# Optimization experiments

Hardware: AMD Instinct MI355X
Metric: run time of the kernel (lower is better)

The kernel has to match this reference:

```python
import jax, jax.numpy as jnp
import numpy as np

NEG_INF = -1e30  # finite stand-in for log(0); keeps grads NaN-free

T_, B_, V_, L_ = 1024, 64, 512, 256


def setup_inputs() -> dict:
    key = jax.random.key(0)
    k1, k2 = jax.random.split(key)
    acts = jax.random.normal(k1, (T_, B_, V_), dtype=jnp.float32)
    labels = jax.random.randint(k2, (B_ * L_,), 1, V_, dtype=jnp.int32)  # blank=0 excluded
    act_lens = jnp.full((B_,), T_, dtype=jnp.int32)
    label_lens = jnp.full((B_,), L_, dtype=jnp.int32)
    return {"acts": acts, "labels": labels, "act_lens": act_lens, "label_lens": label_lens}


def _ctc_total_loss(acts, labels, act_lens, label_lens):
    # acts: (T, B, V) raw logits; warp-ctc applies softmax internally.
    T, B, V = acts.shape
    L = labels.shape[0] // B          # static max label length (uniform lengths)
    S = 2 * L + 1                     # extended label lattice with interleaved blanks
    logp = jax.nn.log_softmax(acts, axis=-1)

    # Unflatten labels -> padded (B, L)
    offsets = jnp.concatenate([jnp.zeros((1,), jnp.int32),
                               jnp.cumsum(label_lens.astype(jnp.int32))])[:-1]
    j = jnp.arange(L, dtype=jnp.int32)
    gidx = jnp.clip(offsets[:, None] + j[None, :], 0, labels.shape[0] - 1)
    padded = jnp.where(j[None, :] < label_lens[:, None], labels[gidx], 0)  # (B, L)

    # Extended labels: blank, l1, blank, l2, ..., blank
    ext = jnp.zeros((B, S), dtype=labels.dtype).at[:, 1::2].set(padded)
    ext_m2 = jnp.pad(ext, ((0, 0), (2, 0)))[:, :S]
    allow_skip = (ext != 0) & (ext != ext_m2)
    allow_skip = allow_skip.at[:, :2].set(False)

    bidx = jnp.arange(B)[:, None]
    lp_ext = logp[:, bidx, ext]       # (T, B, S): per-frame log-prob of lattice states

    alpha0 = jnp.full((B, S), NEG_INF, dtype=acts.dtype)
    alpha0 = alpha0.at[:, 0].set(lp_ext[0, :, 0]).at[:, 1].set(lp_ext[0, :, 1])
    neg = jnp.full((B, 1), NEG_INF, dtype=acts.dtype)

    def step(alpha, inp):
        lp_t, t = inp
        a1 = alpha
        a2 = jnp.concatenate([neg, alpha[:, :-1]], axis=1)
        a3 = jnp.concatenate([neg, neg, alpha[:, :-2]], axis=1)
        a3 = jnp.where(allow_skip, a3, NEG_INF)
        new = lp_t + jnp.logaddexp(jnp.logaddexp(a1, a2), a3)
        alpha = jnp.where((t < act_lens)[:, None], new, alpha)  # freeze past act_len
        return alpha, None

    alpha, _ = jax.lax.scan(step, alpha0, (lp_ext[1:], jnp.arange(1, T)))

    s_end = (2 * label_lens).astype(jnp.int32)           # final blank state
    a_end = jnp.take_along_axis(alpha, s_end[:, None], axis=1)[:, 0]
    a_end2 = jnp.take_along_axis(alpha, jnp.maximum(s_end - 1, 0)[:, None], axis=1)[:, 0]
    losses = -jnp.logaddexp(a_end, a_end2)               # per-example NLL
    return jnp.sum(losses)[None]                         # shape (1,), matches FloatTensor([sum])


def reference(acts, labels, act_lens, label_lens):
    return _ctc_total_loss(acts, labels, act_lens, label_lens)
```

## Files before the change

kernel.cpp:

```cpp
#include <hip/hip_runtime.h>

constexpr int T = 1024;
constexpr int B = 64;
constexpr int V = 512;
constexpr int L = 256;
constexpr int S = 2 * L + 1;
constexpr int C = 16;

typedef float f32x4 __attribute__((ext_vector_type(4)));

__device__ __forceinline__ unsigned short f2bf(float f) {
    unsigned u = __float_as_uint(f);
    u += 0x7fffu + ((u >> 16) & 1u);
    return (unsigned short)(u >> 16);
}


__global__ __launch_bounds__(64) void offsets_kernel(
    const int* __restrict__ label_lens, int* __restrict__ offsets)
{
    int lane = threadIdx.x;
    int v = (lane < B) ? label_lens[lane] : 0;
    int x = v;
#pragma unroll
    for (int o = 1; o < 64; o <<= 1) {
        int y = __shfl_up(x, o, 64);
        if (lane >= o) x += y;
    }
    if (lane < B) offsets[lane] = x - v;
}

__global__ __launch_bounds__(256) void setup_kernel(
    const float* __restrict__ acts, const int* __restrict__ labels,
    const int* __restrict__ label_lens, const int* __restrict__ offsets,
    float* __restrict__ lse_rows, unsigned short* __restrict__ packedU,
    float* __restrict__ blankU)
{
    __shared__ float rows[4][2][V];
    const int w    = threadIdx.x >> 6;
    const int lane = threadIdx.x & 63;
    const int rbase = (blockIdx.x * 4 + w) * 2;
    const f32x4* p = (const f32x4*)(acts + (size_t)rbase * V);

    f32x4 xa0 = __builtin_nontemporal_load(p + lane);
    f32x4 xa1 = __builtin_nontemporal_load(p + lane + 64);
    f32x4 xb0 = __builtin_nontemporal_load(p + lane + 128);
    f32x4 xb1 = __builtin_nontemporal_load(p + lane + 192);
    f32x4 ea0, ea1, eb0, eb1;
    ea0.x=__expf(xa0.x); ea0.y=__expf(xa0.y); ea0.z=__expf(xa0.z); ea0.w=__expf(xa0.w);
    ea1.x=__expf(xa1.x); ea1.y=__expf(xa1.y); ea1.z=__expf(xa1.z); ea1.w=__expf(xa1.w);
    eb0.x=__expf(xb0.x); eb0.y=__expf(xb0.y); eb0.z=__expf(xb0.z); eb0.w=__expf(xb0.w);
    eb1.x=__expf(xb1.x); eb1.y=__expf(xb1.y); eb1.z=__expf(xb1.z); eb1.w=__expf(xb1.w);
    ((f32x4*)rows[w][0])[lane]      = ea0;
    ((f32x4*)rows[w][0])[lane + 64] = ea1;
    ((f32x4*)rows[w][1])[lane]      = eb0;
    ((f32x4*)rows[w][1])[lane + 64] = eb1;
    float sa = ea0.x+ea0.y+ea0.z+ea0.w + ea1.x+ea1.y+ea1.z+ea1.w;
    float sb = eb0.x+eb0.y+eb0.z+eb0.w + eb1.x+eb1.y+eb1.z+eb1.w;
#pragma unroll
    for (int o = 32; o; o >>= 1) { sa += __shfl_xor(sa, o, 64); sb += __shfl_xor(sb, o, 64); }

#pragma unroll
    for (int rr = 0; rr < 2; ++rr) {
        const int r = rbase + rr;
        const int b = r & (B - 1), t = r >> 6;
        const float* rw = rows[w][rr];
        const int lab_len = label_lens[b];
        const int off     = offsets[b];
        const float ubk   = rw[0];
        const int j0 = 4 * lane;
        float q0 = (j0 + 0 < lab_len) ? rw[labels[min(off + j0 + 0, B * L - 1)]] : ubk;
        float q1 = (j0 + 1 < lab_len) ? rw[labels[min(off + j0 + 1, B * L - 1)]] : ubk;
        float q2 = (j0 + 2 < lab_len) ? rw[labels[min(off + j0 + 2, B * L - 1)]] : ubk;
        float q3 = (j0 + 3 < lab_len) ? rw[labels[min(off + j0 + 3, B * L - 1)]] : ubk;
        ushort4 hv = {f2bf(q0), f2bf(q1), f2bf(q2), f2bf(q3)};
        ((ushort4*)packedU)[(size_t)(b * T + t) * 64 + lane] = hv;
        if (lane == 0) {
            lse_rows[b * T + t] = __logf(rr ? sb : sa);
            blankU[b * T + t]   = ubk;
        }
    }
}

__global__ __launch_bounds__(128, 1) void ctc_kernel(
    const int* __restrict__ labels, const int* __restrict__ act_lens,
    const int* __restrict__ label_lens, const int* __restrict__ offsets,
    const float* __restrict__ lse_rows, const unsigned short* __restrict__ packedU,
    const float* __restrict__ blankU, float* __restrict__ out)
{
    __shared__ uint4 ubuf[2][2][C * 32];
    __shared__ float bbuf[2][2][C];
    __shared__ float sbr[S];
    __shared__ float s_accb;

    const int b    = blockIdx.x;
    const int wave = threadIdx.x >> 6;
    const int lane = threadIdx.x & 63;
    const int lab_len = label_lens[b];
    const int a_len   = act_lens[b];
    const int th      = (a_len - 1) >> 1;
    const int off     = offsets[b];
    const size_t rowbase = (size_t)b * T;

    int li0 = 4 * lane;
    int eprev = (li0 - 1 >= 0 && li0 - 1 < lab_len) ? labels[min(off + li0 - 1, B * L - 1)] : 0;
    int enext = (li0 + 4 < lab_len) ? labels[min(off + li0 + 4, B * L - 1)] : 0;
    int e0 = (li0 + 0 < lab_len) ? labels[min(off + li0 + 0, B * L - 1)] : 0;
    int e1 = (li0 + 1 < lab_len) ? labels[min(off + li0 + 1, B * L - 1)] : 0;
    int e2 = (li0 + 2 < lab_len) ? labels[min(off + li0 + 2, B * L - 1)] : 0;
    int e3 = (li0 + 3 < lab_len) ? labels[min(off + li0 + 3, B * L - 1)] : 0;

    const float aF0 = (8 * lane + 1 >= 2 && e0 != 0 && e0 != eprev) ? 1.f : 0.f;
    const float aF1 = (e1 != 0 && e1 != e0) ? 1.f : 0.f;
    const float aF2 = (e2 != 0 && e2 != e1) ? 1.f : 0.f;
    const float aF3 = (e3 != 0 && e3 != e2) ? 1.f : 0.f;
    const float aB0 = aF1, aB1 = aF2, aB2 = aF3;
    const float aB3 = (enext != 0 && enext != e3) ? 1.f : 0.f;

    float A0 = 0.f, A1 = 0.f, A2 = 0.f, A3 = 0.f, A4 = 0.f,
          A5 = 0.f, A6 = 0.f, A7 = 0.f, A8 = 0.f;
    float acc = 0.f, sls = 0.f;
    uint4 G0, G1, G2, G3, G4, G5, G6, G7;
    float BL = 0.f;

#define LOADCHUNK(TLO) do {                                                   \
        const uint4* gp_ = (const uint4*)(packedU + (rowbase + (TLO)) * 256); \
        G0 = gp_[lane];       G1 = gp_[lane + 64];                            \
        G2 = gp_[lane + 128]; G3 = gp_[lane + 192];                           \
        G4 = gp_[lane + 256]; G5 = gp_[lane + 320];                           \
        G6 = gp_[lane + 384]; G7 = gp_[lane + 448];                           \
        if (lane < C) BL = blankU[rowbase + (TLO) + lane];                    \
    } while (0)

#define WRITEBUF(BI) do {                                                     \
        uint4* wp_ = ubuf[wave][BI];                                          \
        wp_[lane] = G0;       wp_[lane + 64] = G1;                            \
        wp_[lane + 128] = G2; wp_[lane + 192] = G3;                           \
        wp_[lane + 256] = G4; wp_[lane + 320] = G5;                           \
        wp_[lane + 384] = G6; wp_[lane + 448] = G7;                           \
        if (lane < C) bbuf[wave][BI][lane] = BL;                              \
    } while (0)

#define RESCALE() do {                                                        \
        float m_ = fmaxf(A8, A0); m_ = fmaxf(m_, A1); m_ = fmaxf(m_, A2);     \
        m_ = fmaxf(m_, A3); m_ = fmaxf(m_, A4); m_ = fmaxf(m_, A5);           \
        m_ = fmaxf(m_, A6); m_ = fmaxf(m_, A7);                               \
        _Pragma("unroll")                                                     \
        for (int o_ = 32; o_; o_ >>= 1) m_ = fmaxf(m_, __shfl_xor(m_, o_, 64)); \
        m_ = fmaxf(m_, 1e-30f);                                               \
        float inv_ = __builtin_amdgcn_rcpf(m_);                               \
        acc += __logf(m_);                                                    \
        A0 *= inv_; A1 *= inv_; A2 *= inv_; A3 *= inv_; A4 *= inv_;           \
        A5 *= inv_; A6 *= inv_; A7 *= inv_; A8 *= inv_;                       \
    } while (0)

#define STEPF(BI, ROW) do {                                                   \
        uint2 hv_ = ((const uint2*)ubuf[wave][BI])[(ROW) * 64 + lane];        \
        float ub_ = bbuf[wave][BI][ROW];                                      \
        float u0_ = __uint_as_float(hv_.x << 16);                             \
        float u1_ = __uint_as_float(hv_.x & 0xffff0000u);                     \
        float u2_ = __uint_as_float(hv_.y << 16);                             \
        float u3_ = __uint_as_float(hv_.y & 0xffff0000u);                     \
        float pA7_ = __shfl_up(A7, 1, 64);                                    \
        if (lane == 0) pA7_ = 0.f;                                            \
        A8 = ub_ * (A8 + A7);                                                 \
        A7 = u3_ * fmaf(aF3, A5, A7 + A6);                                    \
        A6 = ub_ * (A6 + A5);                                                 \
        A5 = u2_ * fmaf(aF2, A3, A5 + A4);                                    \
        A4 = ub_ * (A4 + A3);                                                 \
        A3 = u1_ * fmaf(aF1, A1, A3 + A2);                                    \
        A2 = ub_ * (A2 + A1);                                                 \
        A1 = u0_ * fmaf(aF0, pA7_, A1 + A0);                                  \
        A0 = ub_ * (A0 + pA7_);                                               \
    } while (0)

#define STEPB(BI, ROW) do {                                                   \
        uint2 hv_ = ((const uint2*)ubuf[wave][BI])[(ROW) * 64 + lane];        \
        float ub_ = bbuf[wave][BI][ROW];                                      \
        float u0_ = __uint_as_float(hv_.x << 16);                             \
        float u1_ = __uint_as_float(hv_.x & 0xffff0000u);                     \
        float u2_ = __uint_as_float(hv_.y << 16);                             \
        float u3_ = __uint_as_float(hv_.y & 0xffff0000u);                     \
        float nB0_ = __shfl_down(A0, 1, 64);                                  \
        float nB1_ = __shfl_down(A1, 1, 64);                                  \
        if (lane == 63) { nB0_ = A8; nB1_ = 0.f; }                            \
        A8 = ub_ * A8;                                                        \
        A0 = ub_ * (A0 + A1);                                                 \
        A1 = u0_ * fmaf(aB0, A3, A1 + A2);                                    \
        A2 = ub_ * (A2 + A3);                                                 \
        A3 = u1_ * fmaf(aB1, A5, A3 + A4);                                    \
        A4 = ub_ * (A4 + A5);                                                 \
        A5 = u2_ * fmaf(aB2, A7, A5 + A6);                                    \
        A6 = ub_ * (A6 + A7);                                                 \
        A7 = u3_ * fmaf(aB3, nB1_, A7 + nB0_);                                \
    } while (0)

    if (wave == 0) {
        for (int t = lane; t < a_len; t += 64) sls += lse_rows[rowbase + t];
#pragma unroll
        for (int o = 32; o; o >>= 1) sls += __shfl_xor(sls, o, 64);

        if (lane == 0) {
            A0 = blankU[rowbase];
            A1 = __uint_as_float(((unsigned)packedU[rowbase * 256]) << 16);
        }

        const int nst = th;
        if (nst > 0) {
            const int nc = (nst + C - 1) / C;
            LOADCHUNK(1);
            WRITEBUF(0);
            LOADCHUNK(1 + C * min(1, nc - 1));
            for (int k = 0; k < nc; ++k) {
                const int bi  = k & 1;
                const int tlo = 1 + C * k;
#pragma unroll
                for (int i = 0; i < C; ++i) {
                    if (tlo + i <= th) STEPF(bi, i);
                    if (i == 7 || i == 15) RESCALE();
                }
                WRITEBUF((k + 1) & 1);
                LOADCHUNK(1 + C * min(k + 2, nc - 1));
            }
        }
    } else {
        const int send = 2 * lab_len;
        {
            size_t rl = rowbase + (a_len - 1);
            float ubl = blankU[rl];
            float ue  = (lab_len > 0)
                      ? __uint_as_float(((unsigned)packedU[rl * 256 + (lab_len - 1)]) << 16)
                      : 0.f;
            int s0 = 8 * lane;
            A0 = (s0 + 0 == send) ? ubl : ((s0 + 0 == send - 1) ? ue : 0.f);
            A1 = (s0 + 1 == send) ? ubl : ((s0 + 1 == send - 1) ? ue : 0.f);
            A2 = (s0 + 2 == send) ? ubl : ((s0 + 2 == send - 1) ? ue : 0.f);
            A3 = (s0 + 3 == send) ? ubl : ((s0 + 3 == send - 1) ? ue : 0.f);
            A4 = (s0 + 4 == send) ? ubl : ((s0 + 4 == send - 1) ? ue : 0.f);
            A5 = (s0 + 5 == send) ? ubl : ((s0 + 5 == send - 1) ? ue : 0.f);
            A6 = (s0 + 6 == send) ? ubl : ((s0 + 6 == send - 1) ? ue : 0.f);
            A7 = (s0 + 7 == send) ? ubl : ((s0 + 7 == send - 1) ? ue : 0.f);
            A8 = (lane == 63 && send == 512) ? ubl : 0.f;
        }

        const int nst = a_len - 2 - th;
        if (nst > 0) {
            const int nc = (nst + C - 1) / C;
#define BTLO(K) max(a_len - 2 - C * (K) - (C - 1), 0)
            LOADCHUNK(BTLO(0));
            WRITEBUF(0);
            LOADCHUNK(BTLO(min(1, nc - 1)));
            for (int k = 0; k < nc; ++k) {
                const int bi   = k & 1;
                const int thi  = a_len - 2 - C * k;
                const int tloc = max(thi - (C - 1), 0);
#pragma unroll
                for (int i = 0; i < C; ++i) {
                    int tt = thi - i;
                    if (tt >= th + 1) STEPB(bi, tt - tloc);
                    if (i == 7 || i == 15) RESCALE();
                }
                WRITEBUF((k + 1) & 1);
                LOADCHUNK(BTLO(min(k + 2, nc - 1)));
            }
#undef BTLO
        }

        {
            float nB0 = __shfl_down(A0, 1, 64);
            float nB1 = __shfl_down(A1, 1, 64);
            if (lane == 63) { nB0 = A8; nB1 = 0.f; }
            float w0 = A0 + A1;
            float w1 = fmaf(aB0, A3, A1 + A2);
            float w2 = A2 + A3;
            float w3 = fmaf(aB1, A5, A3 + A4);
            float w4 = A4 + A5;
            float w5 = fmaf(aB2, A7, A5 + A6);
            float w6 = A6 + A7;
            float w7 = fmaf(aB3, nB1, A7 + nB0);
            int s0 = 8 * lane;
            sbr[s0 + 0] = w0; sbr[s0 + 1] = w1; sbr[s0 + 2] = w2; sbr[s0 + 3] = w3;
            sbr[s0 + 4] = w4; sbr[s0 + 5] = w5; sbr[s0 + 6] = w6; sbr[s0 + 7] = w7;
            if (lane == 63) sbr[512] = A8;
            if (lane == 0)  s_accb = acc;
        }
    }
    __syncthreads();
    if (wave == 0) {
        int s0 = 8 * lane;
        float p0 = __logf(fmaxf(A0, 1e-37f)) + __logf(fmaxf(sbr[s0 + 0], 1e-37f));
        float p1 = __logf(fmaxf(A1, 1e-37f)) + __logf(fmaxf(sbr[s0 + 1], 1e-37f));
        float p2 = __logf(fmaxf(A2, 1e-37f)) + __logf(fmaxf(sbr[s0 + 2], 1e-37f));
        float p3 = __logf(fmaxf(A3, 1e-37f)) + __logf(fmaxf(sbr[s0 + 3], 1e-37f));
        float p4 = __logf(fmaxf(A4, 1e-37f)) + __logf(fmaxf(sbr[s0 + 4], 1e-37f));
        float p5 = __logf(fmaxf(A5, 1e-37f)) + __logf(fmaxf(sbr[s0 + 5], 1e-37f));
        float p6 = __logf(fmaxf(A6, 1e-37f)) + __logf(fmaxf(sbr[s0 + 6], 1e-37f));
        float p7 = __logf(fmaxf(A7, 1e-37f)) + __logf(fmaxf(sbr[s0 + 7], 1e-37f));
        float p8 = -3.0e38f;
        if (lane == 63) p8 = __logf(fmaxf(A8, 1e-37f)) + __logf(fmaxf(sbr[512], 1e-37f));
        float pmax = fmaxf(fmaxf(fmaxf(p0, p1), fmaxf(p2, p3)),
                           fmaxf(fmaxf(p4, p5), fmaxf(p6, p7)));
        pmax = fmaxf(pmax, p8);
#pragma unroll
        for (int o = 32; o; o >>= 1) pmax = fmaxf(pmax, __shfl_xor(pmax, o, 64));
        float dot = __expf(p0 - pmax) + __expf(p1 - pmax) + __expf(p2 - pmax)
                  + __expf(p3 - pmax) + __expf(p4 - pmax) + __expf(p5 - pmax)
                  + __expf(p6 - pmax) + __expf(p7 - pmax);
        if (lane == 63) dot += __expf(p8 - pmax);
#pragma unroll
        for (int o = 32; o; o >>= 1) dot += __shfl_xor(dot, o, 64);
        if (lane == 0) {
            float loss = sls - acc - s_accb - (pmax + __logf(dot));
            atomicAdd(out, loss);
        }
    }
#undef LOADCHUNK
#undef WRITEBUF
#undef RESCALE
#undef STEPF
#undef STEPB
}

extern "C" void kernel_launch(void* const* d_in, const int* in_sizes, int n_in,
                              void* d_out, int out_size, void* d_ws, size_t ws_size,
                              hipStream_t stream) {
    const float* acts       = (const float*)d_in[0];
    const int*   labels     = (const int*)d_in[1];
    const int*   act_lens   = (const int*)d_in[2];
    const int*   label_lens = (const int*)d_in[3];
    float*       out        = (float*)d_out;

    float*          lse_rows = (float*)d_ws;
    float*          blankU   = (float*)((char*)d_ws + (size_t)T * B * 4);
    int*            offsets  = (int*)  ((char*)d_ws + (size_t)2 * T * B * 4);
    unsigned short* packedU  = (unsigned short*)((char*)d_ws + (1u << 20));

    hipMemsetAsync(d_out, 0, sizeof(float), stream);

    offsets_kernel<<<1, 64, 0, stream>>>(label_lens, offsets);
    setup_kernel<<<T * B / 8, 256, 0, stream>>>(
        acts, labels, label_lens, offsets, lse_rows, packedU, blankU);
    ctc_kernel<<<B, 128, 0, stream>>>(
        labels, act_lens, label_lens, offsets, lse_rows, packedU, blankU, out);
}
```

Baseline: 279.4 us.

## Stream CTC emission chunks through registers instead of LDS double buffer

Removes the shared-memory staging buffers. Each wave now loads 16-step chunks of packed bf16 emissions directly into two register arrays that ping-pong, and takes the blank probability from a lane via readlane instead of from LDS. The backward recursion's state layout is shifted by one so lane 0 holds the extra state. Chunks are fully unrolled with a remainder loop that reads global memory directly, and rescaling happens once per chunk instead of twice. This trades higher register pressure and extra edge-case complexity for fewer LDS writes and reads on the serial recurrence path.

```diff
diff --git a/kernel.cpp b/kernel.cpp
--- a/kernel.cpp
+++ b/kernel.cpp
@@ -13,6 +13,10 @@
     unsigned u = __float_as_uint(f);
     u += 0x7fffu + ((u >> 16) & 1u);
     return (unsigned short)(u >> 16);
+}
+
+__device__ __forceinline__ float lane_bcast(float v, int i) {
+    return __uint_as_float((unsigned)__builtin_amdgcn_readlane((int)__float_as_uint(v), i));
 }
 
 
@@ -88,8 +92,6 @@
     const float* __restrict__ lse_rows, const unsigned short* __restrict__ packedU,
     const float* __restrict__ blankU, float* __restrict__ out)
 {
-    __shared__ uint4 ubuf[2][2][C * 32];
-    __shared__ float bbuf[2][2][C];
     __shared__ float sbr[S];
     __shared__ float s_accb;
 
@@ -120,25 +122,16 @@
     float A0 = 0.f, A1 = 0.f, A2 = 0.f, A3 = 0.f, A4 = 0.f,
           A5 = 0.f, A6 = 0.f, A7 = 0.f, A8 = 0.f;
     float acc = 0.f, sls = 0.f;
-    uint4 G0, G1, G2, G3, G4, G5, G6, G7;
-    float BL = 0.f;
-
-#define LOADCHUNK(TLO) do {                                                   \
-        const uint4* gp_ = (const uint4*)(packedU + (rowbase + (TLO)) * 256); \
-        G0 = gp_[lane];       G1 = gp_[lane + 64];                            \
-        G2 = gp_[lane + 128]; G3 = gp_[lane + 192];                           \
-        G4 = gp_[lane + 256]; G5 = gp_[lane + 320];                           \
-        G6 = gp_[lane + 384]; G7 = gp_[lane + 448];                           \
-        if (lane < C) BL = blankU[rowbase + (TLO) + lane];                    \
-    } while (0)
-
-#define WRITEBUF(BI) do {                                                     \
-        uint4* wp_ = ubuf[wave][BI];                                          \
-        wp_[lane] = G0;       wp_[lane + 64] = G1;                            \
-        wp_[lane + 128] = G2; wp_[lane + 192] = G3;                           \
-        wp_[lane + 256] = G4; wp_[lane + 320] = G5;                           \
-        wp_[lane + 384] = G6; wp_[lane + 448] = G7;                           \
-        if (lane < C) bbuf[wave][BI][lane] = BL;                              \
+
+    uint2 Ua[C], Ub[C];
+    float Ka = 0.f, Kb = 0.f;
+
+#define LOADCH(U, K, TLO) do {                                                \
+        const int tl_ = min(max((int)(TLO), 0), T - C);                       \
+        const uint2* gp_ = (const uint2*)(packedU + (rowbase + tl_) * 256);   \
+        _Pragma("unroll")                                                     \
+        for (int i_ = 0; i_ < C; ++i_) U[i_] = gp_[i_ * 64 + lane];           \
+        K = blankU[rowbase + tl_ + (lane & (C - 1))];                         \
     } while (0)
 
 #define RESCALE() do {                                                        \
@@ -154,13 +147,13 @@
         A5 *= inv_; A6 *= inv_; A7 *= inv_; A8 *= inv_;                       \
     } while (0)
 
-#define STEPF(BI, ROW) do {                                                   \
-        uint2 hv_ = ((const uint2*)ubuf[wave][BI])[(ROW) * 64 + lane];        \
-        float ub_ = bbuf[wave][BI][ROW];                                      \
-        float u0_ = __uint_as_float(hv_.x << 16);                             \
-        float u1_ = __uint_as_float(hv_.x & 0xffff0000u);                     \
-        float u2_ = __uint_as_float(hv_.y << 16);                             \
-        float u3_ = __uint_as_float(hv_.y & 0xffff0000u);                     \
+#define STEPF_CORE(HX, HY, UB) do {                                           \
+        const float ub_ = (UB);                                               \
+        const unsigned hx_ = (HX), hy_ = (HY);                                \
+        const float u0_ = __uint_as_float(hx_ << 16);                         \
+        const float u1_ = __uint_as_float(hx_ & 0xffff0000u);                 \
+        const float u2_ = __uint_as_float(hy_ << 16);                         \
+        const float u3_ = __uint_as_float(hy_ & 0xffff0000u);                 \
         float pA7_ = __shfl_up(A7, 1, 64);                                    \
         if (lane == 0) pA7_ = 0.f;                                            \
         A8 = ub_ * (A8 + A7);                                                 \
@@ -173,26 +166,33 @@
         A1 = u0_ * fmaf(aF0, pA7_, A1 + A0);                                  \
         A0 = ub_ * (A0 + pA7_);                                               \
     } while (0)
-
-#define STEPB(BI, ROW) do {                                                   \
-        uint2 hv_ = ((const uint2*)ubuf[wave][BI])[(ROW) * 64 + lane];        \
-        float ub_ = bbuf[wave][BI][ROW];                                      \
-        float u0_ = __uint_as_float(hv_.x << 16);                             \
-        float u1_ = __uint_as_float(hv_.x & 0xffff0000u);                     \
-        float u2_ = __uint_as_float(hv_.y << 16);                             \
-        float u3_ = __uint_as_float(hv_.y & 0xffff0000u);                     \
-        float nB0_ = __shfl_down(A0, 1, 64);                                  \
-        float nB1_ = __shfl_down(A1, 1, 64);                                  \
-        if (lane == 63) { nB0_ = A8; nB1_ = 0.f; }                            \
-        A8 = ub_ * A8;                                                        \
-        A0 = ub_ * (A0 + A1);                                                 \
-        A1 = u0_ * fmaf(aB0, A3, A1 + A2);                                    \
-        A2 = ub_ * (A2 + A3);                                                 \
-        A3 = u1_ * fmaf(aB1, A5, A3 + A4);                                    \
-        A4 = ub_ * (A4 + A5);                                                 \
-        A5 = u2_ * fmaf(aB2, A7, A5 + A6);                                    \
-        A6 = ub_ * (A6 + A7);                                                 \
-        A7 = u3_ * fmaf(aB3, nB1_, A7 + nB0_);                                \
+#define STEPF_R(U, K, I) STEPF_CORE(U[I].x, U[I].y, lane_bcast(K, I))
+
+#define STEPB_CORE(HX, HY, UB) do {                                           \
+        const float ub_ = (UB);                                               \
+        const unsigned hx_ = (HX), hy_ = (HY);                                \
+        const float u0_ = __uint_as_float(hx_ << 16);                         \
+        const float u1_ = __uint_as_float(hx_ & 0xffff0000u);                 \
+        const float u2_ = __uint_as_float(hy_ << 16);                         \
+        const float u3_ = __uint_as_float(hy_ & 0xffff0000u);                 \
+        float nC0_ = __shfl_down(A0, 1, 64);                                  \
+        if (lane == 63) nC0_ = 0.f;                                           \
+        A8 = ub_ * (A8 + A0);                                                 \
+        A0 = u0_ * fmaf(aB0, A2, A0 + A1);                                    \
+        A1 = ub_ * (A1 + A2);                                                 \
+        A2 = u1_ * fmaf(aB1, A4, A2 + A3);                                    \
+        A3 = ub_ * (A3 + A4);                                                 \
+        A4 = u2_ * fmaf(aB2, A6, A4 + A5);                                    \
+        A5 = ub_ * (A5 + A6);                                                 \
+        A6 = u3_ * fmaf(aB3, nC0_, A6 + A7);                                  \
+        A7 = ub_ * (A7 + nC0_);                                               \
+    } while (0)
+#define STEPB_R(U, K, I) STEPB_CORE(U[I].x, U[I].y, lane_bcast(K, I))
+
+#define STEP_DIRECT(WHICH, TT) do {                                           \
+        uint2 hvd_ = ((const uint2*)(packedU + (rowbase + (TT)) * 256))[lane];\
+        float ubd_ = blankU[rowbase + (TT)];                                  \
+        WHICH(hvd_.x, hvd_.y, ubd_);                                          \
     } while (0)
 
     if (wave == 0) {
@@ -205,22 +205,34 @@
             A1 = __uint_as_float(((unsigned)packedU[rowbase * 256]) << 16);
         }
 
-        const int nst = th;
-        if (nst > 0) {
-            const int nc = (nst + C - 1) / C;
-            LOADCHUNK(1);
-            WRITEBUF(0);
-            LOADCHUNK(1 + C * min(1, nc - 1));
-            for (int k = 0; k < nc; ++k) {
-                const int bi  = k & 1;
-                const int tlo = 1 + C * k;
-#pragma unroll
-                for (int i = 0; i < C; ++i) {
-                    if (tlo + i <= th) STEPF(bi, i);
-                    if (i == 7 || i == 15) RESCALE();
-                }
-                WRITEBUF((k + 1) & 1);
-                LOADCHUNK(1 + C * min(k + 2, nc - 1));
+        if (th >= 1) {
+            const int kfull = (th - 15) >> 4;
+            LOADCH(Ua, Ka, 0);
+            LOADCH(Ub, Kb, 16);
+#pragma unroll
+            for (int i = 1; i < C; ++i) { if (i <= th) STEPF_R(Ua, Ka, i); }
+            RESCALE();
+            LOADCH(Ua, Ka, 32);
+            int k = 1;
+            for (; k + 1 <= kfull; k += 2) {
+#pragma unroll
+                for (int i = 0; i < C; ++i) STEPF_R(Ub, Kb, i);
+                RESCALE();
+                LOADCH(Ub, Kb, 16 * (k + 2));
+#pragma unroll
+                for (int i = 0; i < C; ++i) STEPF_R(Ua, Ka, i);
+                RESCALE();
+                LOADCH(Ua, Ka, 16 * (k + 3));
+            }
+            if (k <= kfull) {
+#pragma unroll
+                for (int i = 0; i < C; ++i) STEPF_R(Ub, Kb, i);
+                RESCALE();
+            }
+            const int tS = (kfull >= 1) ? 16 * (kfull + 1) : 16;
+            for (int t = tS; t <= th; ++t) {
+                STEP_DIRECT(STEPF_CORE, t);
+                if (((t - tS) & 7) == 7) RESCALE();
             }
         }
     } else {
@@ -231,7 +243,7 @@
             float ue  = (lab_len > 0)
                       ? __uint_as_float(((unsigned)packedU[rl * 256 + (lab_len - 1)]) << 16)
                       : 0.f;
-            int s0 = 8 * lane;
+            int s0 = 8 * lane + 1;
             A0 = (s0 + 0 == send) ? ubl : ((s0 + 0 == send - 1) ? ue : 0.f);
             A1 = (s0 + 1 == send) ? ubl : ((s0 + 1 == send - 1) ? ue : 0.f);
             A2 = (s0 + 2 == send) ? ubl : ((s0 + 2 == send - 1) ? ue : 0.f);
@@ -240,49 +252,65 @@
             A5 = (s0 + 5 == send) ? ubl : ((s0 + 5 == send - 1) ? ue : 0.f);
             A6 = (s0 + 6 == send) ? ubl : ((s0 + 6 == send - 1) ? ue : 0.f);
             A7 = (s0 + 7 == send) ? ubl : ((s0 + 7 == send - 1) ? ue : 0.f);
-            A8 = (lane == 63 && send == 512) ? ubl : 0.f;
-        }
-
-        const int nst = a_len - 2 - th;
-        if (nst > 0) {
-            const int nc = (nst + C - 1) / C;
-#define BTLO(K) max(a_len - 2 - C * (K) - (C - 1), 0)
-            LOADCHUNK(BTLO(0));
-            WRITEBUF(0);
-            LOADCHUNK(BTLO(min(1, nc - 1)));
-            for (int k = 0; k < nc; ++k) {
-                const int bi   = k & 1;
-                const int thi  = a_len - 2 - C * k;
-                const int tloc = max(thi - (C - 1), 0);
-#pragma unroll
-                for (int i = 0; i < C; ++i) {
-                    int tt = thi - i;
-                    if (tt >= th + 1) STEPB(bi, tt - tloc);
-                    if (i == 7 || i == 15) RESCALE();
-                }
-                WRITEBUF((k + 1) & 1);
-                LOADCHUNK(BTLO(min(k + 2, nc - 1)));
-            }
-#undef BTLO
+            A8 = (send == 0) ? ubl : 0.f;
+        }
+
+        const int nstB = a_len - 2 - th;
+        if (nstB > 0 && a_len >= 16) {
+            const int cfull = (a_len - th - 17) >> 4;
+            LOADCH(Ua, Ka, a_len - 16);
+            LOADCH(Ub, Kb, a_len - 32);
+#pragma unroll
+            for (int i = C - 2; i >= 0; --i) {
+                if (a_len - 16 + i >= th + 1) STEPB_R(Ua, Ka, i);
+            }
+            RESCALE();
+            LOADCH(Ua, Ka, a_len - 48);
+            int c = 1;
+            for (; c + 1 <= cfull; c += 2) {
+#pragma unroll
+                for (int i = C - 1; i >= 0; --i) STEPB_R(Ub, Kb, i);
+                RESCALE();
+                LOADCH(Ub, Kb, a_len - 16 * (c + 3));
+#pragma unroll
+                for (int i = C - 1; i >= 0; --i) STEPB_R(Ua, Ka, i);
+                RESCALE();
+                LOADCH(Ua, Ka, a_len - 16 * (c + 4));
+            }
+            if (c <= cfull) {
+#pragma unroll
+                for (int i = C - 1; i >= 0; --i) STEPB_R(Ub, Kb, i);
+                RESCALE();
+            }
+            const int cf = (cfull >= 1) ? cfull : 0;
+            const int tE = a_len - 16 * (cf + 1) - 1;
+            for (int t = tE; t >= th + 1; --t) {
+                STEP_DIRECT(STEPB_CORE, t);
+                if (((tE - t) & 7) == 7) RESCALE();
+            }
+        } else if (nstB > 0) {
+            for (int t = a_len - 2; t >= th + 1; --t) {
+                STEP_DIRECT(STEPB_CORE, t);
+                if (((a_len - 2 - t) & 7) == 7) RESCALE();
+            }
         }
 
         {
-            float nB0 = __shfl_down(A0, 1, 64);
-            float nB1 = __shfl_down(A1, 1, 64);
-            if (lane == 63) { nB0 = A8; nB1 = 0.f; }
-            float w0 = A0 + A1;
-            float w1 = fmaf(aB0, A3, A1 + A2);
-            float w2 = A2 + A3;
-            float w3 = fmaf(aB1, A5, A3 + A4);
-            float w4 = A4 + A5;
-            float w5 = fmaf(aB2, A7, A5 + A6);
-            float w6 = A6 + A7;
-            float w7 = fmaf(aB3, nB1, A7 + nB0);
-            int s0 = 8 * lane;
-            sbr[s0 + 0] = w0; sbr[s0 + 1] = w1; sbr[s0 + 2] = w2; sbr[s0 + 3] = w3;
-            sbr[s0 + 4] = w4; sbr[s0 + 5] = w5; sbr[s0 + 6] = w6; sbr[s0 + 7] = w7;
-            if (lane == 63) sbr[512] = A8;
-            if (lane == 0)  s_accb = acc;
+            float nC0 = __shfl_down(A0, 1, 64);
+            if (lane == 63) nC0 = 0.f;
+            float w1 = fmaf(aB0, A2, A0 + A1);
+            float w2 = A1 + A2;
+            float w3 = fmaf(aB1, A4, A2 + A3);
+            float w4 = A3 + A4;
+            float w5 = fmaf(aB2, A6, A4 + A5);
+            float w6 = A5 + A6;
+            float w7 = fmaf(aB3, nC0, A6 + A7);
+            float w8 = A7 + nC0;
+            int sB = 8 * lane + 1;
+            sbr[sB + 0] = w1; sbr[sB + 1] = w2; sbr[sB + 2] = w3; sbr[sB + 3] = w4;
+            sbr[sB + 4] = w5; sbr[sB + 5] = w6; sbr[sB + 6] = w7; sbr[sB + 7] = w8;
+            if (lane == 0) sbr[0] = A8 + A0;
+            if (lane == 0) s_accb = acc;
         }
     }
     __syncthreads();
@@ -314,11 +342,13 @@
             atomicAdd(out, loss);
         }
     }
-#undef LOADCHUNK
-#undef WRITEBUF
+#undef LOADCH
 #undef RESCALE
-#undef STEPF
-#undef STEPB
+#undef STEPF_CORE
+#undef STEPF_R
+#undef STEPB_CORE
+#undef STEPB_R
+#undef STEP_DIRECT
 }
 
 extern "C" void kernel_launch(void* const* d_in, const int* in_sizes, int n_in,
```

Measured after the change: 250.4 us. 10.4% less time.
